# Kernel tuning notes

Measured on AMD Instinct MI355X. Metric: run time of the kernel, lower is better.

## Reference

```python
import jax, jax.numpy as jnp
import numpy as np

N = 100000   # nodes
E = 1600000  # edges
F_IN = 32    # num_features
H = 16       # hidden_size (hardcoded as conv2 input in source)
C = 10       # num_classes
K = 2        # kernel_size (dim=1)


def setup_inputs() -> dict:
    key = jax.random.key(0)
    ks = jax.random.split(key, 9)
    x = jax.random.normal(ks[0], (N, F_IN), dtype=jnp.float32)
    edge_index = jax.random.randint(ks[1], (2, E), 0, N, dtype=jnp.int64)
    edge_attr = jax.random.uniform(ks[2], (E, 1), dtype=jnp.float32)
    s1 = 1.0 / np.sqrt(F_IN)
    s2 = 1.0 / np.sqrt(H)
    W1 = jax.random.normal(ks[3], (K, F_IN, H), dtype=jnp.float32) * s1
    root1 = jax.random.normal(ks[4], (F_IN, H), dtype=jnp.float32) * s1
    b1 = jnp.zeros((H,), dtype=jnp.float32)
    W2 = jax.random.normal(ks[5], (K, H, C), dtype=jnp.float32) * s2
    root2 = jax.random.normal(ks[6], (H, C), dtype=jnp.float32) * s2
    b2 = jnp.zeros((C,), dtype=jnp.float32)
    return {"x": x, "edge_index": edge_index, "edge_attr": edge_attr,
            "W1": W1, "root1": root1, "b1": b1,
            "W2": W2, "root2": root2, "b2": b2}


def spline_conv(x, edge_index, edge_attr, W, root, bias, num_nodes):
    # Open B-spline, degree 1: hat-function basis over K knots.
    k = W.shape[0]
    src, dst = edge_index[0], edge_index[1]
    v = edge_attr[:, 0] * (k - 1)                                   # [E]
    grid = jnp.arange(k, dtype=v.dtype)
    basis = jnp.maximum(0.0, 1.0 - jnp.abs(v[:, None] - grid[None, :]))  # [E,K]
    xe = x[src]                                                      # [E,in] gather
    msg = jnp.einsum('ei,kio,ek->eo', xe, W, basis)                  # per-edge message
    agg = jax.ops.segment_sum(msg, dst, num_segments=num_nodes)      # scatter-add
    deg = jax.ops.segment_sum(jnp.ones((msg.shape[0],), x.dtype), dst,
                              num_segments=num_nodes)
    agg = agg / jnp.maximum(deg, 1.0)[:, None]                       # mean aggregation
    return agg + x @ root + bias


def reference(x, edge_index, edge_attr, W1, root1, b1, W2, root2, b2):
    # Inference mode: F.dropout(training=False) is identity.
    h = jax.nn.elu(spline_conv(x, edge_index, edge_attr, W1, root1, b1, N))
    out = spline_conv(h, edge_index, edge_attr, W2, root2, b2, N)
    return jax.nn.log_softmax(out, axis=1)
```

## Files before the change

kernel.cpp:

```cpp
#include <hip/hip_runtime.h>
#include <math.h>

#define N_NODES 100000
#define E_EDGES 1600000
#define F_IN 32
#define HID 16
#define NC 10
#define SRC_BITS 17
#define SRC_MASK ((1u << SRC_BITS) - 1u)
#define VQ_SCALE 32767.0f
#define CBITS 8
#define BUCKET_N 256
#define NCB ((N_NODES + BUCKET_N - 1) / BUCKET_N)
#define BLK_E 2048
#define NBLK ((E_EDGES + BLK_E - 1) / BLK_E)
#define NODE_GRID ((N_NODES + 255) / 256)

__device__ __forceinline__ unsigned int bf16pair(float lo, float hi) {
    unsigned int ulo = __float_as_uint(lo), uhi = __float_as_uint(hi);
    ulo += 0x7fffu + ((ulo >> 16) & 1u);
    uhi += 0x7fffu + ((uhi >> 16) & 1u);
    return (ulo >> 16) | (uhi & 0xffff0000u);
}

__device__ __forceinline__ float lerp_pair(unsigned int pair, float v) {
    float a = __uint_as_float(pair << 16);
    float b = __uint_as_float(pair & 0xffff0000u);
    return fmaf(v, b - a, a);
}

__global__ __launch_bounds__(256) void fused_l1cnt(
    const float* __restrict__ x, const float* __restrict__ W1,
    const float* __restrict__ root1, const float* __restrict__ b1,
    const int* __restrict__ ei,
    unsigned int* __restrict__ y, float* __restrict__ r1,
    int* __restrict__ cnt)
{
    if (blockIdx.x >= NODE_GRID) {
        __shared__ int h[NCB];
        int b = blockIdx.x - NODE_GRID;
        for (int i = threadIdx.x; i < NCB; i += 256) h[i] = 0;
        __syncthreads();
        const int* dstp = ei + E_EDGES;
        int e0 = b * BLK_E;
        for (int i = threadIdx.x * 4; i < BLK_E; i += 1024) {
            int e = e0 + i;
            if (e + 3 < E_EDGES) {
                int4 d4 = *(const int4*)(dstp + e);
                atomicAdd(&h[d4.x >> CBITS], 1);
                atomicAdd(&h[d4.y >> CBITS], 1);
                atomicAdd(&h[d4.z >> CBITS], 1);
                atomicAdd(&h[d4.w >> CBITS], 1);
            } else {
                for (int k = 0; k < 4; k++)
                    if (e + k < E_EDGES) atomicAdd(&h[dstp[e + k] >> CBITS], 1);
            }
        }
        __syncthreads();
        for (int s = threadIdx.x; s < NCB; s += 256)
            cnt[(size_t)s * NBLK + b] = h[s];
        return;
    }
    __shared__ float sW0[F_IN * HID], sW1[F_IN * HID], sR[F_IN * HID], sB[HID];
    for (int i = threadIdx.x; i < F_IN * HID; i += 256) {
        sW0[i] = W1[i];
        sW1[i] = W1[F_IN * HID + i];
        sR[i]  = root1[i];
    }
    if (threadIdx.x < HID) sB[threadIdx.x] = b1[threadIdx.x];
    __syncthreads();

    int n = blockIdx.x * 256 + threadIdx.x;
    if (n >= N_NODES) return;

    float xr[F_IN];
    const float4* xp = (const float4*)(x + (size_t)n * F_IN);
    #pragma unroll
    for (int i = 0; i < F_IN / 4; i++) {
        float4 t = xp[i];
        xr[i*4+0] = t.x; xr[i*4+1] = t.y; xr[i*4+2] = t.z; xr[i*4+3] = t.w;
    }

    float a0[HID], a1[HID], ar[HID];
    #pragma unroll
    for (int o = 0; o < HID; o++) { a0[o] = 0.f; a1[o] = 0.f; ar[o] = sB[o]; }
    for (int i = 0; i < F_IN; i++) {
        float xi = xr[i];
        #pragma unroll
        for (int o = 0; o < HID; o++) {
            a0[o] += xi * sW0[i * HID + o];
            a1[o] += xi * sW1[i * HID + o];
            ar[o] += xi * sR[i * HID + o];
        }
    }
    unsigned int* py = y + (size_t)n * 16;
    float* pr = r1 + (size_t)n * HID;
    #pragma unroll
    for (int o = 0; o < HID; o++) {
        py[o] = bf16pair(a0[o], a1[o]);
        pr[o] = ar[o];
    }
}

__global__ __launch_bounds__(256) void k_rowscan(
    int* __restrict__ cnt, int* __restrict__ total)
{
    __shared__ int wsum[4], woff[4];
    int s = blockIdx.x;
    int t = threadIdx.x;
    int w = t >> 6, l = t & 63;
    int carry = 0;
    int* row = cnt + (size_t)s * NBLK;
    for (int c = 0; c < NBLK; c += 256) {
        int idx = c + t;
        int v = (idx < NBLK) ? row[idx] : 0;
        int incl = v;
        #pragma unroll
        for (int off = 1; off < 64; off <<= 1) {
            int u = __shfl_up(incl, off, 64);
            if (l >= off) incl += u;
        }
        if (l == 63) wsum[w] = incl;
        __syncthreads();
        if (t == 0) {
            int a = 0;
            #pragma unroll
            for (int i = 0; i < 4; i++) { woff[i] = a; a += wsum[i]; }
        }
        __syncthreads();
        int excl = woff[w] + incl - v;
        if (idx < NBLK) row[idx] = carry + excl;
        carry += woff[3] + wsum[3];
        __syncthreads();
    }
    if (t == 0) total[s] = carry;
}

__global__ __launch_bounds__(512) void k_bucket(
    const int* __restrict__ ei, const float* __restrict__ ea,
    const int* __restrict__ cnt, const int* __restrict__ total,
    int2* __restrict__ ebuf, int* __restrict__ bb, int* __restrict__ start)
{
    __shared__ int wsum[8], woff[8];
    __shared__ int base[NCB], cur[NCB];
    int t = threadIdx.x;
    int tot = (t < NCB) ? total[t] : 0;
    int w = t >> 6, l = t & 63;
    int incl = tot;
    #pragma unroll
    for (int off = 1; off < 64; off <<= 1) {
        int u = __shfl_up(incl, off, 64);
        if (l >= off) incl += u;
    }
    if (l == 63) wsum[w] = incl;
    __syncthreads();
    if (t == 0) {
        int a = 0;
        #pragma unroll
        for (int i = 0; i < 8; i++) { woff[i] = a; a += wsum[i]; }
    }
    __syncthreads();
    int excl = woff[w] + incl - tot;
    if (t < NCB) {
        base[t] = excl + cnt[(size_t)t * NBLK + blockIdx.x];
        cur[t] = 0;
        if (blockIdx.x == 0) {
            bb[t] = excl;
            if (t == NCB - 1) { bb[NCB] = excl + tot; start[N_NODES] = E_EDGES; }
        }
    }
    __syncthreads();

    const int* dstp = ei + E_EDGES;
    int e0 = blockIdx.x * BLK_E;
    for (int i = t * 4; i < BLK_E; i += 2048) {
        int e = e0 + i;
        if (e + 3 < E_EDGES) {
            int4 d4 = *(const int4*)(dstp + e);
            int4 s4 = *(const int4*)(ei + e);
            float4 a4 = *(const float4*)(ea + e);
            {
                int s = d4.x >> CBITS;
                int off = atomicAdd(&cur[s], 1);
                unsigned int vq = (unsigned int)(a4.x * VQ_SCALE + 0.5f);
                ebuf[base[s] + off] = make_int2(d4.x & (BUCKET_N - 1),
                                               (int)((vq << SRC_BITS) | (unsigned int)s4.x));
            }
            {
                int s = d4.y >> CBITS;
                int off = atomicAdd(&cur[s], 1);
                unsigned int vq = (unsigned int)(a4.y * VQ_SCALE + 0.5f);
                ebuf[base[s] + off] = make_int2(d4.y & (BUCKET_N - 1),
                                               (int)((vq << SRC_BITS) | (unsigned int)s4.y));
            }
            {
                int s = d4.z >> CBITS;
                int off = atomicAdd(&cur[s], 1);
                unsigned int vq = (unsigned int)(a4.z * VQ_SCALE + 0.5f);
                ebuf[base[s] + off] = make_int2(d4.z & (BUCKET_N - 1),
                                               (int)((vq << SRC_BITS) | (unsigned int)s4.z));
            }
            {
                int s = d4.w >> CBITS;
                int off = atomicAdd(&cur[s], 1);
                unsigned int vq = (unsigned int)(a4.w * VQ_SCALE + 0.5f);
                ebuf[base[s] + off] = make_int2(d4.w & (BUCKET_N - 1),
                                               (int)((vq << SRC_BITS) | (unsigned int)s4.w));
            }
        } else {
            for (int k = 0; k < 4; k++) {
                int ee = e + k;
                if (ee >= E_EDGES) break;
                int dst = dstp[ee];
                int s = dst >> CBITS;
                int off = atomicAdd(&cur[s], 1);
                unsigned int vq = (unsigned int)(ea[ee] * VQ_SCALE + 0.5f);
                ebuf[base[s] + off] = make_int2(dst & (BUCKET_N - 1),
                                               (int)((vq << SRC_BITS) | (unsigned int)ei[ee]));
            }
        }
    }
}

__global__ __launch_bounds__(1024) void k_bsort(
    const int2* __restrict__ ebuf, const int* __restrict__ bb,
    unsigned int* __restrict__ es, int* __restrict__ start)
{
    __shared__ int hist[BUCKET_N];
    __shared__ int cursor[BUCKET_N];
    __shared__ int wsum[4], woff[4];
    int t = threadIdx.x;
    int b = blockIdx.x;
    int j0 = bb[b], j1 = bb[b + 1];
    if (t < BUCKET_N) { hist[t] = 0; cursor[t] = 0; }
    __syncthreads();
    for (int j = j0 + t; j < j1; j += 1024)
        atomicAdd(&hist[ebuf[j].x], 1);
    __syncthreads();
    int c = (t < BUCKET_N) ? hist[t] : 0;
    int w = t >> 6, l = t & 63;
    int incl = c;
    #pragma unroll
    for (int off = 1; off < 64; off <<= 1) {
        int u = __shfl_up(incl, off, 64);
        if (l >= off) incl += u;
    }
    if (w < 4 && l == 63) wsum[w] = incl;
    __syncthreads();
    if (t == 0) {
        int acc = 0;
        #pragma unroll
        for (int i = 0; i < 4; i++) { woff[i] = acc; acc += wsum[i]; }
    }
    __syncthreads();
    if (t < BUCKET_N) {
        int excl = woff[w] + incl - c;
        hist[t] = excl;
        int node = (b << CBITS) + t;
        if (node < N_NODES) start[node] = j0 + excl;
    }
    __syncthreads();
    for (int j = j0 + t; j < j1; j += 1024) {
        int2 p = ebuf[j];
        int off = atomicAdd(&cursor[p.x], 1);
        es[j0 + hist[p.x] + off] = (unsigned int)p.y;
    }
}

__global__ __launch_bounds__(256) void k_agg1(
    const unsigned int* __restrict__ es, const int* __restrict__ start,
    const unsigned int* __restrict__ y, const float* __restrict__ r1,
    const float* __restrict__ W2, const float* __restrict__ root2,
    const float* __restrict__ b2,
    unsigned int* __restrict__ z, float* __restrict__ r2)
{
    __shared__ float sh[16 * 17];
    __shared__ float sW0[HID * NC], sW1[HID * NC], sRt[HID * NC], sB2[NC];
    int t = threadIdx.x;
    if (t < HID * NC) { sW0[t] = W2[t]; sW1[t] = W2[HID * NC + t]; sRt[t] = root2[t]; }
    if (t >= HID * NC && t < HID * NC + NC) sB2[t - HID * NC] = b2[t - HID * NC];

    int idx = blockIdx.x * 256 + t;
    int n = idx >> 4, o = idx & 15, g = t >> 4;
    if (n < N_NODES) {
        int j0 = start[n], j1 = start[n + 1];
        float acc0 = 0.f, acc1 = 0.f, acc2 = 0.f, acc3 = 0.f;
        int j = j0;
        for (; j + 7 < j1; j += 8) {
            unsigned int p0 = es[j],   p1 = es[j+1], p2 = es[j+2], p3 = es[j+3];
            unsigned int p4 = es[j+4], p5 = es[j+5], p6 = es[j+6], p7 = es[j+7];
            unsigned int q0 = y[(size_t)(p0 & SRC_MASK) * 16 + o];
            unsigned int q1 = y[(size_t)(p1 & SRC_MASK) * 16 + o];
            unsigned int q2 = y[(size_t)(p2 & SRC_MASK) * 16 + o];
            unsigned int q3 = y[(size_t)(p3 & SRC_MASK) * 16 + o];
            unsigned int q4 = y[(size_t)(p4 & SRC_MASK) * 16 + o];
            unsigned int q5 = y[(size_t)(p5 & SRC_MASK) * 16 + o];
            unsigned int q6 = y[(size_t)(p6 & SRC_MASK) * 16 + o];
            unsigned int q7 = y[(size_t)(p7 & SRC_MASK) * 16 + o];
            acc0 += lerp_pair(q0, (float)(p0 >> SRC_BITS) * (1.0f / VQ_SCALE));
            acc1 += lerp_pair(q1, (float)(p1 >> SRC_BITS) * (1.0f / VQ_SCALE));
            acc2 += lerp_pair(q2, (float)(p2 >> SRC_BITS) * (1.0f / VQ_SCALE));
            acc3 += lerp_pair(q3, (float)(p3 >> SRC_BITS) * (1.0f / VQ_SCALE));
            acc0 += lerp_pair(q4, (float)(p4 >> SRC_BITS) * (1.0f / VQ_SCALE));
            acc1 += lerp_pair(q5, (float)(p5 >> SRC_BITS) * (1.0f / VQ_SCALE));
            acc2 += lerp_pair(q6, (float)(p6 >> SRC_BITS) * (1.0f / VQ_SCALE));
            acc3 += lerp_pair(q7, (float)(p7 >> SRC_BITS) * (1.0f / VQ_SCALE));
        }
        for (; j + 3 < j1; j += 4) {
            unsigned int p0 = es[j], p1 = es[j+1], p2 = es[j+2], p3 = es[j+3];
            unsigned int q0 = y[(size_t)(p0 & SRC_MASK) * 16 + o];
            unsigned int q1 = y[(size_t)(p1 & SRC_MASK) * 16 + o];
            unsigned int q2 = y[(size_t)(p2 & SRC_MASK) * 16 + o];
            unsigned int q3 = y[(size_t)(p3 & SRC_MASK) * 16 + o];
            acc0 += lerp_pair(q0, (float)(p0 >> SRC_BITS) * (1.0f / VQ_SCALE));
            acc1 += lerp_pair(q1, (float)(p1 >> SRC_BITS) * (1.0f / VQ_SCALE));
            acc2 += lerp_pair(q2, (float)(p2 >> SRC_BITS) * (1.0f / VQ_SCALE));
            acc3 += lerp_pair(q3, (float)(p3 >> SRC_BITS) * (1.0f / VQ_SCALE));
        }
        for (; j < j1; j++) {
            unsigned int p = es[j];
            unsigned int q = y[(size_t)(p & SRC_MASK) * 16 + o];
            acc0 += lerp_pair(q, (float)(p >> SRC_BITS) * (1.0f / VQ_SCALE));
        }
        float acc = (acc0 + acc1) + (acc2 + acc3);
        float inv = 1.0f / fmaxf((float)(j1 - j0), 1.0f);
        float hv = acc * inv + r1[(size_t)n * HID + o];
        sh[g * 17 + o] = hv > 0.0f ? hv : expm1f(hv);
    }
    __syncthreads();

    int n2 = blockIdx.x * 16 + g;
    if (n2 < N_NODES) {
        int cc = o;
        unsigned int* pz = z + (size_t)n2 * 16;
        if (cc < NC) {
            float a0 = 0.f, a1 = 0.f, ar = sB2[cc];
            #pragma unroll
            for (int i = 0; i < HID; i++) {
                float hi = sh[g * 17 + i];
                a0 += hi * sW0[i * NC + cc];
                a1 += hi * sW1[i * NC + cc];
                ar += hi * sRt[i * NC + cc];
            }
            pz[cc] = bf16pair(a0, a1);
            r2[(size_t)n2 * NC + cc] = ar;
        } else {
            pz[cc] = 0u;
        }
    }
}

__global__ __launch_bounds__(256) void k_agg2(
    const unsigned int* __restrict__ es, const int* __restrict__ start,
    const unsigned int* __restrict__ z,
    const float* __restrict__ r2, float* __restrict__ out)
{
    int idx = blockIdx.x * 256 + threadIdx.x;
    int n = idx >> 4, o = idx & 15;
    if (n >= N_NODES) return;
    int j0 = start[n], j1 = start[n + 1];
    float acc0 = 0.f, acc1 = 0.f, acc2 = 0.f, acc3 = 0.f;
    int j = j0;
    for (; j + 7 < j1; j += 8) {
        unsigned int p0 = es[j],   p1 = es[j+1], p2 = es[j+2], p3 = es[j+3];
        unsigned int p4 = es[j+4], p5 = es[j+5], p6 = es[j+6], p7 = es[j+7];
        unsigned int q0 = z[(size_t)(p0 & SRC_MASK) * 16 + o];
        unsigned int q1 = z[(size_t)(p1 & SRC_MASK) * 16 + o];
        unsigned int q2 = z[(size_t)(p2 & SRC_MASK) * 16 + o];
        unsigned int q3 = z[(size_t)(p3 & SRC_MASK) * 16 + o];
        unsigned int q4 = z[(size_t)(p4 & SRC_MASK) * 16 + o];
        unsigned int q5 = z[(size_t)(p5 & SRC_MASK) * 16 + o];
        unsigned int q6 = z[(size_t)(p6 & SRC_MASK) * 16 + o];
        unsigned int q7 = z[(size_t)(p7 & SRC_MASK) * 16 + o];
        acc0 += lerp_pair(q0, (float)(p0 >> SRC_BITS) * (1.0f / VQ_SCALE));
        acc1 += lerp_pair(q1, (float)(p1 >> SRC_BITS) * (1.0f / VQ_SCALE));
        acc2 += lerp_pair(q2, (float)(p2 >> SRC_BITS) * (1.0f / VQ_SCALE));
        acc3 += lerp_pair(q3, (float)(p3 >> SRC_BITS) * (1.0f / VQ_SCALE));
        acc0 += lerp_pair(q4, (float)(p4 >> SRC_BITS) * (1.0f / VQ_SCALE));
        acc1 += lerp_pair(q5, (float)(p5 >> SRC_BITS) * (1.0f / VQ_SCALE));
        acc2 += lerp_pair(q6, (float)(p6 >> SRC_BITS) * (1.0f / VQ_SCALE));
        acc3 += lerp_pair(q7, (float)(p7 >> SRC_BITS) * (1.0f / VQ_SCALE));
    }
    for (; j + 3 < j1; j += 4) {
        unsigned int p0 = es[j], p1 = es[j+1], p2 = es[j+2], p3 = es[j+3];
        unsigned int q0 = z[(size_t)(p0 & SRC_MASK) * 16 + o];
        unsigned int q1 = z[(size_t)(p1 & SRC_MASK) * 16 + o];
        unsigned int q2 = z[(size_t)(p2 & SRC_MASK) * 16 + o];
        unsigned int q3 = z[(size_t)(p3 & SRC_MASK) * 16 + o];
        acc0 += lerp_pair(q0, (float)(p0 >> SRC_BITS) * (1.0f / VQ_SCALE));
        acc1 += lerp_pair(q1, (float)(p1 >> SRC_BITS) * (1.0f / VQ_SCALE));
        acc2 += lerp_pair(q2, (float)(p2 >> SRC_BITS) * (1.0f / VQ_SCALE));
        acc3 += lerp_pair(q3, (float)(p3 >> SRC_BITS) * (1.0f / VQ_SCALE));
    }
    for (; j < j1; j++) {
        unsigned int p = es[j];
        unsigned int q = z[(size_t)(p & SRC_MASK) * 16 + o];
        acc0 += lerp_pair(q, (float)(p >> SRC_BITS) * (1.0f / VQ_SCALE));
    }
    float acc = (acc0 + acc1) + (acc2 + acc3);
    float val = -INFINITY;
    if (o < NC) {
        float inv = 1.0f / fmaxf((float)(j1 - j0), 1.0f);
        val = acc * inv + r2[(size_t)n * NC + o];
    }
    float mx = val;
    #pragma unroll
    for (int off = 8; off > 0; off >>= 1) mx = fmaxf(mx, __shfl_xor(mx, off, 16));
    float ex = (o < NC) ? expf(val - mx) : 0.0f;
    float ssum = ex;
    #pragma unroll
    for (int off = 8; off > 0; off >>= 1) ssum += __shfl_xor(ssum, off, 16);
    if (o < NC) out[(size_t)n * NC + o] = val - mx - logf(ssum);
}

extern "C" void kernel_launch(void* const* d_in, const int* in_sizes, int n_in,
                              void* d_out, int out_size, void* d_ws, size_t ws_size,
                              hipStream_t stream) {
    const float* x     = (const float*)d_in[0];
    const int*   ei    = (const int*)d_in[1];
    const float* ea    = (const float*)d_in[2];
    const float* W1    = (const float*)d_in[3];
    const float* root1 = (const float*)d_in[4];
    const float* b1    = (const float*)d_in[5];
    const float* W2    = (const float*)d_in[6];
    const float* root2 = (const float*)d_in[7];
    const float* b2    = (const float*)d_in[8];
    float* out = (float*)d_out;

    char* wsb = (char*)d_ws;
    int2*         ebuf   = (int2*)wsb;
    unsigned int* es     = (unsigned int*)(wsb + (size_t)E_EDGES * 8);
    unsigned int* y      = es + (size_t)E_EDGES;
    float*        r1     = (float*)(y + (size_t)N_NODES * 16);
    unsigned int* z      = (unsigned int*)(r1 + (size_t)N_NODES * HID);
    float*        r2     = (float*)(z + (size_t)N_NODES * 16);
    int*          start  = (int*)(r2 + (size_t)N_NODES * NC);
    int*          cnt    = start + N_NODES + 1;
    int*          total  = cnt + (size_t)NCB * NBLK;
    int*          bb     = total + NCB;

    int aggGrid  = (N_NODES * 16 + 255) / 256;

    fused_l1cnt<<<NODE_GRID + NBLK, 256, 0, stream>>>(x, W1, root1, b1, ei, y, r1, cnt);
    k_rowscan<<<NCB, 256, 0, stream>>>(cnt, total);
    k_bucket<<<NBLK, 512, 0, stream>>>(ei, ea, cnt, total, ebuf, bb, start);
    k_bsort <<<NCB, 1024, 0, stream>>>(ebuf, bb, es, start);
    k_agg1  <<<aggGrid, 256, 0, stream>>>(es, start, y, r1, W2, root2, b2, z, r2);
    k_agg2  <<<aggGrid, 256, 0, stream>>>(es, start, z, r2, out);
}
```

Before: 185.5 us.

## Drop per-node CSR sort; aggregate each destination bucket in shared memory

```diff
diff --git a/kernel.cpp b/kernel.cpp
--- a/kernel.cpp
+++ b/kernel.cpp
@@ -9,8 +9,8 @@
 #define SRC_BITS 17
 #define SRC_MASK ((1u << SRC_BITS) - 1u)
 #define VQ_SCALE 32767.0f
-#define CBITS 8
-#define BUCKET_N 256
+#define CBITS 7
+#define BUCKET_N 128
 #define NCB ((N_NODES + BUCKET_N - 1) / BUCKET_N)
 #define BLK_E 2048
 #define NBLK ((E_EDGES + BLK_E - 1) / BLK_E)
@@ -139,36 +139,40 @@
 __global__ __launch_bounds__(512) void k_bucket(
     const int* __restrict__ ei, const float* __restrict__ ea,
     const int* __restrict__ cnt, const int* __restrict__ total,
-    int2* __restrict__ ebuf, int* __restrict__ bb, int* __restrict__ start)
+    int2* __restrict__ ebuf, int* __restrict__ bb)
 {
     __shared__ int wsum[8], woff[8];
     __shared__ int base[NCB], cur[NCB];
     int t = threadIdx.x;
-    int tot = (t < NCB) ? total[t] : 0;
     int w = t >> 6, l = t & 63;
-    int incl = tot;
-    #pragma unroll
-    for (int off = 1; off < 64; off <<= 1) {
-        int u = __shfl_up(incl, off, 64);
-        if (l >= off) incl += u;
-    }
-    if (l == 63) wsum[w] = incl;
-    __syncthreads();
-    if (t == 0) {
-        int a = 0;
-        #pragma unroll
-        for (int i = 0; i < 8; i++) { woff[i] = a; a += wsum[i]; }
-    }
-    __syncthreads();
-    int excl = woff[w] + incl - tot;
-    if (t < NCB) {
-        base[t] = excl + cnt[(size_t)t * NBLK + blockIdx.x];
-        cur[t] = 0;
-        if (blockIdx.x == 0) {
-            bb[t] = excl;
-            if (t == NCB - 1) { bb[NCB] = excl + tot; start[N_NODES] = E_EDGES; }
-        }
-    }
+    int carry = 0;
+    for (int c = 0; c < NCB; c += 512) {
+        int idx = c + t;
+        int v = (idx < NCB) ? total[idx] : 0;
+        int incl = v;
+        #pragma unroll
+        for (int off = 1; off < 64; off <<= 1) {
+            int u = __shfl_up(incl, off, 64);
+            if (l >= off) incl += u;
+        }
+        if (l == 63) wsum[w] = incl;
+        __syncthreads();
+        if (t == 0) {
+            int a = 0;
+            #pragma unroll
+            for (int i = 0; i < 8; i++) { woff[i] = a; a += wsum[i]; }
+        }
+        __syncthreads();
+        if (idx < NCB) {
+            int excl = carry + woff[w] + incl - v;
+            base[idx] = excl + cnt[(size_t)idx * NBLK + blockIdx.x];
+            cur[idx] = 0;
+            if (blockIdx.x == 0) bb[idx] = excl;
+        }
+        carry += woff[7] + wsum[7];
+        __syncthreads();
+    }
+    if (blockIdx.x == 0 && t == 0) bb[NCB] = carry;
     __syncthreads();
 
     const int* dstp = ei + E_EDGES;
@@ -222,195 +226,109 @@
     }
 }
 
-__global__ __launch_bounds__(1024) void k_bsort(
+__global__ __launch_bounds__(512) void k_bagg1(
     const int2* __restrict__ ebuf, const int* __restrict__ bb,
-    unsigned int* __restrict__ es, int* __restrict__ start)
-{
-    __shared__ int hist[BUCKET_N];
-    __shared__ int cursor[BUCKET_N];
-    __shared__ int wsum[4], woff[4];
-    int t = threadIdx.x;
-    int b = blockIdx.x;
-    int j0 = bb[b], j1 = bb[b + 1];
-    if (t < BUCKET_N) { hist[t] = 0; cursor[t] = 0; }
-    __syncthreads();
-    for (int j = j0 + t; j < j1; j += 1024)
-        atomicAdd(&hist[ebuf[j].x], 1);
-    __syncthreads();
-    int c = (t < BUCKET_N) ? hist[t] : 0;
-    int w = t >> 6, l = t & 63;
-    int incl = c;
-    #pragma unroll
-    for (int off = 1; off < 64; off <<= 1) {
-        int u = __shfl_up(incl, off, 64);
-        if (l >= off) incl += u;
-    }
-    if (w < 4 && l == 63) wsum[w] = incl;
-    __syncthreads();
-    if (t == 0) {
-        int acc = 0;
-        #pragma unroll
-        for (int i = 0; i < 4; i++) { woff[i] = acc; acc += wsum[i]; }
-    }
-    __syncthreads();
-    if (t < BUCKET_N) {
-        int excl = woff[w] + incl - c;
-        hist[t] = excl;
-        int node = (b << CBITS) + t;
-        if (node < N_NODES) start[node] = j0 + excl;
-    }
-    __syncthreads();
-    for (int j = j0 + t; j < j1; j += 1024) {
-        int2 p = ebuf[j];
-        int off = atomicAdd(&cursor[p.x], 1);
-        es[j0 + hist[p.x] + off] = (unsigned int)p.y;
-    }
-}
-
-__global__ __launch_bounds__(256) void k_agg1(
-    const unsigned int* __restrict__ es, const int* __restrict__ start,
     const unsigned int* __restrict__ y, const float* __restrict__ r1,
     const float* __restrict__ W2, const float* __restrict__ root2,
     const float* __restrict__ b2,
-    unsigned int* __restrict__ z, float* __restrict__ r2)
-{
-    __shared__ float sh[16 * 17];
+    unsigned int* __restrict__ z, float* __restrict__ r2,
+    float* __restrict__ invdeg)
+{
+    __shared__ float acc[BUCKET_N * 16];
+    __shared__ int sdeg[BUCKET_N];
     __shared__ float sW0[HID * NC], sW1[HID * NC], sRt[HID * NC], sB2[NC];
     int t = threadIdx.x;
+    int b = blockIdx.x;
+    for (int i = t; i < BUCKET_N * 16; i += 512) acc[i] = 0.f;
+    if (t < BUCKET_N) sdeg[t] = 0;
     if (t < HID * NC) { sW0[t] = W2[t]; sW1[t] = W2[HID * NC + t]; sRt[t] = root2[t]; }
     if (t >= HID * NC && t < HID * NC + NC) sB2[t - HID * NC] = b2[t - HID * NC];
-
-    int idx = blockIdx.x * 256 + t;
-    int n = idx >> 4, o = idx & 15, g = t >> 4;
-    if (n < N_NODES) {
-        int j0 = start[n], j1 = start[n + 1];
-        float acc0 = 0.f, acc1 = 0.f, acc2 = 0.f, acc3 = 0.f;
-        int j = j0;
-        for (; j + 7 < j1; j += 8) {
-            unsigned int p0 = es[j],   p1 = es[j+1], p2 = es[j+2], p3 = es[j+3];
-            unsigned int p4 = es[j+4], p5 = es[j+5], p6 = es[j+6], p7 = es[j+7];
-            unsigned int q0 = y[(size_t)(p0 & SRC_MASK) * 16 + o];
-            unsigned int q1 = y[(size_t)(p1 & SRC_MASK) * 16 + o];
-            unsigned int q2 = y[(size_t)(p2 & SRC_MASK) * 16 + o];
-            unsigned int q3 = y[(size_t)(p3 & SRC_MASK) * 16 + o];
-            unsigned int q4 = y[(size_t)(p4 & SRC_MASK) * 16 + o];
-            unsigned int q5 = y[(size_t)(p5 & SRC_MASK) * 16 + o];
-            unsigned int q6 = y[(size_t)(p6 & SRC_MASK) * 16 + o];
-            unsigned int q7 = y[(size_t)(p7 & SRC_MASK) * 16 + o];
-            acc0 += lerp_pair(q0, (float)(p0 >> SRC_BITS) * (1.0f / VQ_SCALE));
-            acc1 += lerp_pair(q1, (float)(p1 >> SRC_BITS) * (1.0f / VQ_SCALE));
-            acc2 += lerp_pair(q2, (float)(p2 >> SRC_BITS) * (1.0f / VQ_SCALE));
-            acc3 += lerp_pair(q3, (float)(p3 >> SRC_BITS) * (1.0f / VQ_SCALE));
-            acc0 += lerp_pair(q4, (float)(p4 >> SRC_BITS) * (1.0f / VQ_SCALE));
-            acc1 += lerp_pair(q5, (float)(p5 >> SRC_BITS) * (1.0f / VQ_SCALE));
-            acc2 += lerp_pair(q6, (float)(p6 >> SRC_BITS) * (1.0f / VQ_SCALE));
-            acc3 += lerp_pair(q7, (float)(p7 >> SRC_BITS) * (1.0f / VQ_SCALE));
-        }
-        for (; j + 3 < j1; j += 4) {
-            unsigned int p0 = es[j], p1 = es[j+1], p2 = es[j+2], p3 = es[j+3];
-            unsigned int q0 = y[(size_t)(p0 & SRC_MASK) * 16 + o];
-            unsigned int q1 = y[(size_t)(p1 & SRC_MASK) * 16 + o];
-            unsigned int q2 = y[(size_t)(p2 & SRC_MASK) * 16 + o];
-            unsigned int q3 = y[(size_t)(p3 & SRC_MASK) * 16 + o];
-            acc0 += lerp_pair(q0, (float)(p0 >> SRC_BITS) * (1.0f / VQ_SCALE));
-            acc1 += lerp_pair(q1, (float)(p1 >> SRC_BITS) * (1.0f / VQ_SCALE));
-            acc2 += lerp_pair(q2, (float)(p2 >> SRC_BITS) * (1.0f / VQ_SCALE));
-            acc3 += lerp_pair(q3, (float)(p3 >> SRC_BITS) * (1.0f / VQ_SCALE));
-        }
-        for (; j < j1; j++) {
-            unsigned int p = es[j];
-            unsigned int q = y[(size_t)(p & SRC_MASK) * 16 + o];
-            acc0 += lerp_pair(q, (float)(p >> SRC_BITS) * (1.0f / VQ_SCALE));
-        }
-        float acc = (acc0 + acc1) + (acc2 + acc3);
-        float inv = 1.0f / fmaxf((float)(j1 - j0), 1.0f);
-        float hv = acc * inv + r1[(size_t)n * HID + o];
-        sh[g * 17 + o] = hv > 0.0f ? hv : expm1f(hv);
-    }
-    __syncthreads();
-
-    int n2 = blockIdx.x * 16 + g;
-    if (n2 < N_NODES) {
-        int cc = o;
-        unsigned int* pz = z + (size_t)n2 * 16;
-        if (cc < NC) {
-            float a0 = 0.f, a1 = 0.f, ar = sB2[cc];
-            #pragma unroll
-            for (int i = 0; i < HID; i++) {
-                float hi = sh[g * 17 + i];
-                a0 += hi * sW0[i * NC + cc];
-                a1 += hi * sW1[i * NC + cc];
-                ar += hi * sRt[i * NC + cc];
-            }
-            pz[cc] = bf16pair(a0, a1);
-            r2[(size_t)n2 * NC + cc] = ar;
-        } else {
-            pz[cc] = 0u;
-        }
-    }
-}
-
-__global__ __launch_bounds__(256) void k_agg2(
-    const unsigned int* __restrict__ es, const int* __restrict__ start,
-    const unsigned int* __restrict__ z,
-    const float* __restrict__ r2, float* __restrict__ out)
-{
-    int idx = blockIdx.x * 256 + threadIdx.x;
-    int n = idx >> 4, o = idx & 15;
-    if (n >= N_NODES) return;
-    int j0 = start[n], j1 = start[n + 1];
-    float acc0 = 0.f, acc1 = 0.f, acc2 = 0.f, acc3 = 0.f;
-    int j = j0;
-    for (; j + 7 < j1; j += 8) {
-        unsigned int p0 = es[j],   p1 = es[j+1], p2 = es[j+2], p3 = es[j+3];
-        unsigned int p4 = es[j+4], p5 = es[j+5], p6 = es[j+6], p7 = es[j+7];
-        unsigned int q0 = z[(size_t)(p0 & SRC_MASK) * 16 + o];
-        unsigned int q1 = z[(size_t)(p1 & SRC_MASK) * 16 + o];
-        unsigned int q2 = z[(size_t)(p2 & SRC_MASK) * 16 + o];
-        unsigned int q3 = z[(size_t)(p3 & SRC_MASK) * 16 + o];
-        unsigned int q4 = z[(size_t)(p4 & SRC_MASK) * 16 + o];
-        unsigned int q5 = z[(size_t)(p5 & SRC_MASK) * 16 + o];
-        unsigned int q6 = z[(size_t)(p6 & SRC_MASK) * 16 + o];
-        unsigned int q7 = z[(size_t)(p7 & SRC_MASK) * 16 + o];
-        acc0 += lerp_pair(q0, (float)(p0 >> SRC_BITS) * (1.0f / VQ_SCALE));
-        acc1 += lerp_pair(q1, (float)(p1 >> SRC_BITS) * (1.0f / VQ_SCALE));
-        acc2 += lerp_pair(q2, (float)(p2 >> SRC_BITS) * (1.0f / VQ_SCALE));
-        acc3 += lerp_pair(q3, (float)(p3 >> SRC_BITS) * (1.0f / VQ_SCALE));
-        acc0 += lerp_pair(q4, (float)(p4 >> SRC_BITS) * (1.0f / VQ_SCALE));
-        acc1 += lerp_pair(q5, (float)(p5 >> SRC_BITS) * (1.0f / VQ_SCALE));
-        acc2 += lerp_pair(q6, (float)(p6 >> SRC_BITS) * (1.0f / VQ_SCALE));
-        acc3 += lerp_pair(q7, (float)(p7 >> SRC_BITS) * (1.0f / VQ_SCALE));
-    }
-    for (; j + 3 < j1; j += 4) {
-        unsigned int p0 = es[j], p1 = es[j+1], p2 = es[j+2], p3 = es[j+3];
-        unsigned int q0 = z[(size_t)(p0 & SRC_MASK) * 16 + o];
-        unsigned int q1 = z[(size_t)(p1 & SRC_MASK) * 16 + o];
-        unsigned int q2 = z[(size_t)(p2 & SRC_MASK) * 16 + o];
-        unsigned int q3 = z[(size_t)(p3 & SRC_MASK) * 16 + o];
-        acc0 += lerp_pair(q0, (float)(p0 >> SRC_BITS) * (1.0f / VQ_SCALE));
-        acc1 += lerp_pair(q1, (float)(p1 >> SRC_BITS) * (1.0f / VQ_SCALE));
-        acc2 += lerp_pair(q2, (float)(p2 >> SRC_BITS) * (1.0f / VQ_SCALE));
-        acc3 += lerp_pair(q3, (float)(p3 >> SRC_BITS) * (1.0f / VQ_SCALE));
-    }
-    for (; j < j1; j++) {
-        unsigned int p = es[j];
-        unsigned int q = z[(size_t)(p & SRC_MASK) * 16 + o];
-        acc0 += lerp_pair(q, (float)(p >> SRC_BITS) * (1.0f / VQ_SCALE));
-    }
-    float acc = (acc0 + acc1) + (acc2 + acc3);
-    float val = -INFINITY;
-    if (o < NC) {
-        float inv = 1.0f / fmaxf((float)(j1 - j0), 1.0f);
-        val = acc * inv + r2[(size_t)n * NC + o];
-    }
-    float mx = val;
-    #pragma unroll
-    for (int off = 8; off > 0; off >>= 1) mx = fmaxf(mx, __shfl_xor(mx, off, 16));
-    float ex = (o < NC) ? expf(val - mx) : 0.0f;
-    float ssum = ex;
-    #pragma unroll
-    for (int off = 8; off > 0; off >>= 1) ssum += __shfl_xor(ssum, off, 16);
-    if (o < NC) out[(size_t)n * NC + o] = val - mx - logf(ssum);
+    __syncthreads();
+
+    int j0 = bb[b], j1 = bb[b + 1];
+    int o = t & 15;
+    #pragma unroll 4
+    for (int j = j0 + (t >> 4); j < j1; j += 32) {
+        int2 p = ebuf[j];
+        unsigned int pe = (unsigned int)p.y;
+        float v = (float)(pe >> SRC_BITS) * (1.0f / VQ_SCALE);
+        unsigned int q = y[(size_t)(pe & SRC_MASK) * 16 + o];
+        atomicAdd(&acc[p.x * 16 + o], lerp_pair(q, v));
+        if (o == 0) atomicAdd(&sdeg[p.x], 1);
+    }
+    __syncthreads();
+
+    for (int n = t >> 4; n < BUCKET_N; n += 32) {
+        int node = b * BUCKET_N + n;
+        if (node < N_NODES) {
+            float inv = 1.0f / fmaxf((float)sdeg[n], 1.0f);
+            float hv = acc[n * 16 + o] * inv + r1[(size_t)node * HID + o];
+            acc[n * 16 + o] = hv > 0.0f ? hv : expm1f(hv);
+            if (o == 0) invdeg[node] = inv;
+        }
+    }
+    __syncthreads();
+
+    for (int n = t >> 4; n < BUCKET_N; n += 32) {
+        int node = b * BUCKET_N + n;
+        if (node < N_NODES) {
+            unsigned int* pz = z + (size_t)node * 16;
+            if (o < NC) {
+                float a0 = 0.f, a1 = 0.f, ar = sB2[o];
+                #pragma unroll
+                for (int i = 0; i < HID; i++) {
+                    float hi = acc[n * 16 + i];
+                    a0 += hi * sW0[i * NC + o];
+                    a1 += hi * sW1[i * NC + o];
+                    ar += hi * sRt[i * NC + o];
+                }
+                pz[o] = bf16pair(a0, a1);
+                r2[(size_t)node * NC + o] = ar;
+            } else {
+                pz[o] = 0u;
+            }
+        }
+    }
+}
+
+__global__ __launch_bounds__(512) void k_bagg2(
+    const int2* __restrict__ ebuf, const int* __restrict__ bb,
+    const unsigned int* __restrict__ z, const float* __restrict__ r2,
+    const float* __restrict__ invdeg, float* __restrict__ out)
+{
+    __shared__ float acc[BUCKET_N * 16];
+    int t = threadIdx.x;
+    int b = blockIdx.x;
+    for (int i = t; i < BUCKET_N * 16; i += 512) acc[i] = 0.f;
+    __syncthreads();
+
+    int j0 = bb[b], j1 = bb[b + 1];
+    int o = t & 15;
+    #pragma unroll 4
+    for (int j = j0 + (t >> 4); j < j1; j += 32) {
+        int2 p = ebuf[j];
+        unsigned int pe = (unsigned int)p.y;
+        float v = (float)(pe >> SRC_BITS) * (1.0f / VQ_SCALE);
+        unsigned int q = z[(size_t)(pe & SRC_MASK) * 16 + o];
+        atomicAdd(&acc[p.x * 16 + o], lerp_pair(q, v));
+    }
+    __syncthreads();
+
+    for (int n = t >> 4; n < BUCKET_N; n += 32) {
+        int node = b * BUCKET_N + n;
+        if (node >= N_NODES) continue;
+        float val = -INFINITY;
+        if (o < NC)
+            val = acc[n * 16 + o] * invdeg[node] + r2[(size_t)node * NC + o];
+        float mx = val;
+        #pragma unroll
+        for (int off = 8; off > 0; off >>= 1) mx = fmaxf(mx, __shfl_xor(mx, off, 16));
+        float ex = (o < NC) ? expf(val - mx) : 0.0f;
+        float ssum = ex;
+        #pragma unroll
+        for (int off = 8; off > 0; off >>= 1) ssum += __shfl_xor(ssum, off, 16);
+        if (o < NC) out[(size_t)node * NC + o] = val - mx - logf(ssum);
+    }
 }
 
 extern "C" void kernel_launch(void* const* d_in, const int* in_sizes, int n_in,
@@ -429,22 +347,18 @@
 
     char* wsb = (char*)d_ws;
     int2*         ebuf   = (int2*)wsb;
-    unsigned int* es     = (unsigned int*)(wsb + (size_t)E_EDGES * 8);
-    unsigned int* y      = es + (size_t)E_EDGES;
+    unsigned int* y      = (unsigned int*)(wsb + (size_t)E_EDGES * 8);
     float*        r1     = (float*)(y + (size_t)N_NODES * 16);
     unsigned int* z      = (unsigned int*)(r1 + (size_t)N_NODES * HID);
     float*        r2     = (float*)(z + (size_t)N_NODES * 16);
-    int*          start  = (int*)(r2 + (size_t)N_NODES * NC);
-    int*          cnt    = start + N_NODES + 1;
+    float*        invdeg = r2 + (size_t)N_NODES * NC;
+    int*          cnt    = (int*)(invdeg + N_NODES);
     int*          total  = cnt + (size_t)NCB * NBLK;
     int*          bb     = total + NCB;
 
-    int aggGrid  = (N_NODES * 16 + 255) / 256;
-
     fused_l1cnt<<<NODE_GRID + NBLK, 256, 0, stream>>>(x, W1, root1, b1, ei, y, r1, cnt);
     k_rowscan<<<NCB, 256, 0, stream>>>(cnt, total);
-    k_bucket<<<NBLK, 512, 0, stream>>>(ei, ea, cnt, total, ebuf, bb, start);
-    k_bsort <<<NCB, 1024, 0, stream>>>(ebuf, bb, es, start);
-    k_agg1  <<<aggGrid, 256, 0, stream>>>(es, start, y, r1, W2, root2, b2, z, r2);
-    k_agg2  <<<aggGrid, 256, 0, stream>>>(es, start, z, r2, out);
-}
+    k_bucket<<<NBLK, 512, 0, stream>>>(ei, ea, cnt, total, ebuf, bb);
+    k_bagg1 <<<NCB, 512, 0, stream>>>(ebuf, bb, y, r1, W2, root2, b2, z, r2, invdeg);
+    k_bagg2 <<<NCB, 512, 0, stream>>>(ebuf, bb, z, r2, invdeg, out);
+}
```

New measurement: 491.2 us. +164.8%, slower.

## Use 4 threads per node with 16-byte vector gathers in aggregation kernels

Applied to the files above, without the earlier changes.

```diff
diff --git a/kernel.cpp b/kernel.cpp
--- a/kernel.cpp
+++ b/kernel.cpp
@@ -274,79 +274,86 @@
     const float* __restrict__ b2,
     unsigned int* __restrict__ z, float* __restrict__ r2)
 {
-    __shared__ float sh[16 * 17];
     __shared__ float sW0[HID * NC], sW1[HID * NC], sRt[HID * NC], sB2[NC];
     int t = threadIdx.x;
     if (t < HID * NC) { sW0[t] = W2[t]; sW1[t] = W2[HID * NC + t]; sRt[t] = root2[t]; }
     if (t >= HID * NC && t < HID * NC + NC) sB2[t - HID * NC] = b2[t - HID * NC];
+    __syncthreads();
 
     int idx = blockIdx.x * 256 + t;
-    int n = idx >> 4, o = idx & 15, g = t >> 4;
-    if (n < N_NODES) {
-        int j0 = start[n], j1 = start[n + 1];
-        float acc0 = 0.f, acc1 = 0.f, acc2 = 0.f, acc3 = 0.f;
-        int j = j0;
-        for (; j + 7 < j1; j += 8) {
-            unsigned int p0 = es[j],   p1 = es[j+1], p2 = es[j+2], p3 = es[j+3];
-            unsigned int p4 = es[j+4], p5 = es[j+5], p6 = es[j+6], p7 = es[j+7];
-            unsigned int q0 = y[(size_t)(p0 & SRC_MASK) * 16 + o];
-            unsigned int q1 = y[(size_t)(p1 & SRC_MASK) * 16 + o];
-            unsigned int q2 = y[(size_t)(p2 & SRC_MASK) * 16 + o];
-            unsigned int q3 = y[(size_t)(p3 & SRC_MASK) * 16 + o];
-            unsigned int q4 = y[(size_t)(p4 & SRC_MASK) * 16 + o];
-            unsigned int q5 = y[(size_t)(p5 & SRC_MASK) * 16 + o];
-            unsigned int q6 = y[(size_t)(p6 & SRC_MASK) * 16 + o];
-            unsigned int q7 = y[(size_t)(p7 & SRC_MASK) * 16 + o];
-            acc0 += lerp_pair(q0, (float)(p0 >> SRC_BITS) * (1.0f / VQ_SCALE));
-            acc1 += lerp_pair(q1, (float)(p1 >> SRC_BITS) * (1.0f / VQ_SCALE));
-            acc2 += lerp_pair(q2, (float)(p2 >> SRC_BITS) * (1.0f / VQ_SCALE));
-            acc3 += lerp_pair(q3, (float)(p3 >> SRC_BITS) * (1.0f / VQ_SCALE));
-            acc0 += lerp_pair(q4, (float)(p4 >> SRC_BITS) * (1.0f / VQ_SCALE));
-            acc1 += lerp_pair(q5, (float)(p5 >> SRC_BITS) * (1.0f / VQ_SCALE));
-            acc2 += lerp_pair(q6, (float)(p6 >> SRC_BITS) * (1.0f / VQ_SCALE));
-            acc3 += lerp_pair(q7, (float)(p7 >> SRC_BITS) * (1.0f / VQ_SCALE));
-        }
-        for (; j + 3 < j1; j += 4) {
-            unsigned int p0 = es[j], p1 = es[j+1], p2 = es[j+2], p3 = es[j+3];
-            unsigned int q0 = y[(size_t)(p0 & SRC_MASK) * 16 + o];
-            unsigned int q1 = y[(size_t)(p1 & SRC_MASK) * 16 + o];
-            unsigned int q2 = y[(size_t)(p2 & SRC_MASK) * 16 + o];
-            unsigned int q3 = y[(size_t)(p3 & SRC_MASK) * 16 + o];
-            acc0 += lerp_pair(q0, (float)(p0 >> SRC_BITS) * (1.0f / VQ_SCALE));
-            acc1 += lerp_pair(q1, (float)(p1 >> SRC_BITS) * (1.0f / VQ_SCALE));
-            acc2 += lerp_pair(q2, (float)(p2 >> SRC_BITS) * (1.0f / VQ_SCALE));
-            acc3 += lerp_pair(q3, (float)(p3 >> SRC_BITS) * (1.0f / VQ_SCALE));
-        }
-        for (; j < j1; j++) {
-            unsigned int p = es[j];
-            unsigned int q = y[(size_t)(p & SRC_MASK) * 16 + o];
-            acc0 += lerp_pair(q, (float)(p >> SRC_BITS) * (1.0f / VQ_SCALE));
-        }
-        float acc = (acc0 + acc1) + (acc2 + acc3);
-        float inv = 1.0f / fmaxf((float)(j1 - j0), 1.0f);
-        float hv = acc * inv + r1[(size_t)n * HID + o];
-        sh[g * 17 + o] = hv > 0.0f ? hv : expm1f(hv);
-    }
-    __syncthreads();
-
-    int n2 = blockIdx.x * 16 + g;
-    if (n2 < N_NODES) {
-        int cc = o;
-        unsigned int* pz = z + (size_t)n2 * 16;
-        if (cc < NC) {
-            float a0 = 0.f, a1 = 0.f, ar = sB2[cc];
+    int n = idx >> 2, l = idx & 3;
+    if (n >= N_NODES) return;
+    int j0 = start[n], j1 = start[n + 1];
+    const uint4* yrow = (const uint4*)y;
+    float acc[4] = {0.f, 0.f, 0.f, 0.f};
+    int j = j0;
+    for (; j + 3 < j1; j += 4) {
+        unsigned int p0 = es[j], p1 = es[j+1], p2 = es[j+2], p3 = es[j+3];
+        uint4 q0 = yrow[(size_t)(p0 & SRC_MASK) * 4 + l];
+        uint4 q1 = yrow[(size_t)(p1 & SRC_MASK) * 4 + l];
+        uint4 q2 = yrow[(size_t)(p2 & SRC_MASK) * 4 + l];
+        uint4 q3 = yrow[(size_t)(p3 & SRC_MASK) * 4 + l];
+        float v0 = (float)(p0 >> SRC_BITS) * (1.0f / VQ_SCALE);
+        float v1 = (float)(p1 >> SRC_BITS) * (1.0f / VQ_SCALE);
+        float v2 = (float)(p2 >> SRC_BITS) * (1.0f / VQ_SCALE);
+        float v3 = (float)(p3 >> SRC_BITS) * (1.0f / VQ_SCALE);
+        acc[0] += lerp_pair(q0.x, v0); acc[1] += lerp_pair(q0.y, v0);
+        acc[2] += lerp_pair(q0.z, v0); acc[3] += lerp_pair(q0.w, v0);
+        acc[0] += lerp_pair(q1.x, v1); acc[1] += lerp_pair(q1.y, v1);
+        acc[2] += lerp_pair(q1.z, v1); acc[3] += lerp_pair(q1.w, v1);
+        acc[0] += lerp_pair(q2.x, v2); acc[1] += lerp_pair(q2.y, v2);
+        acc[2] += lerp_pair(q2.z, v2); acc[3] += lerp_pair(q2.w, v2);
+        acc[0] += lerp_pair(q3.x, v3); acc[1] += lerp_pair(q3.y, v3);
+        acc[2] += lerp_pair(q3.z, v3); acc[3] += lerp_pair(q3.w, v3);
+    }
+    for (; j < j1; j++) {
+        unsigned int p = es[j];
+        uint4 q = yrow[(size_t)(p & SRC_MASK) * 4 + l];
+        float v = (float)(p >> SRC_BITS) * (1.0f / VQ_SCALE);
+        acc[0] += lerp_pair(q.x, v); acc[1] += lerp_pair(q.y, v);
+        acc[2] += lerp_pair(q.z, v); acc[3] += lerp_pair(q.w, v);
+    }
+    float inv = 1.0f / fmaxf((float)(j1 - j0), 1.0f);
+    float4 rr = *(const float4*)(r1 + (size_t)n * HID + l * 4);
+    float hv[4];
+    hv[0] = acc[0] * inv + rr.x;
+    hv[1] = acc[1] * inv + rr.y;
+    hv[2] = acc[2] * inv + rr.z;
+    hv[3] = acc[3] * inv + rr.w;
+    #pragma unroll
+    for (int e = 0; e < 4; e++) hv[e] = hv[e] > 0.0f ? hv[e] : expm1f(hv[e]);
+
+    int cbase = l * 4;
+    float a0[4] = {0.f, 0.f, 0.f, 0.f}, a1[4] = {0.f, 0.f, 0.f, 0.f}, ar[4];
+    #pragma unroll
+    for (int e = 0; e < 4; e++) { int c = cbase + e; ar[e] = (c < NC) ? sB2[c] : 0.f; }
+    #pragma unroll
+    for (int s = 0; s < 4; s++) {
+        #pragma unroll
+        for (int e2 = 0; e2 < 4; e2++) {
+            float hi = __shfl(hv[e2], s, 4);
+            int i = s * 4 + e2;
             #pragma unroll
-            for (int i = 0; i < HID; i++) {
-                float hi = sh[g * 17 + i];
-                a0 += hi * sW0[i * NC + cc];
-                a1 += hi * sW1[i * NC + cc];
-                ar += hi * sRt[i * NC + cc];
-            }
-            pz[cc] = bf16pair(a0, a1);
-            r2[(size_t)n2 * NC + cc] = ar;
-        } else {
-            pz[cc] = 0u;
-        }
+            for (int e = 0; e < 4; e++) {
+                int c = cbase + e;
+                if (c < NC) {
+                    a0[e] += hi * sW0[i * NC + c];
+                    a1[e] += hi * sW1[i * NC + c];
+                    ar[e] += hi * sRt[i * NC + c];
+                }
+            }
+        }
+    }
+    uint4 zo;
+    zo.x = (cbase + 0 < NC) ? bf16pair(a0[0], a1[0]) : 0u;
+    zo.y = (cbase + 1 < NC) ? bf16pair(a0[1], a1[1]) : 0u;
+    zo.z = (cbase + 2 < NC) ? bf16pair(a0[2], a1[2]) : 0u;
+    zo.w = (cbase + 3 < NC) ? bf16pair(a0[3], a1[3]) : 0u;
+    ((uint4*)z)[(size_t)n * 4 + l] = zo;
+    #pragma unroll
+    for (int e = 0; e < 4; e++) {
+        int c = cbase + e;
+        if (c < NC) r2[(size_t)n * NC + c] = ar[e];
     }
 }
 
@@ -356,61 +363,63 @@
     const float* __restrict__ r2, float* __restrict__ out)
 {
     int idx = blockIdx.x * 256 + threadIdx.x;
-    int n = idx >> 4, o = idx & 15;
+    int n = idx >> 2, l = idx & 3;
     if (n >= N_NODES) return;
     int j0 = start[n], j1 = start[n + 1];
-    float acc0 = 0.f, acc1 = 0.f, acc2 = 0.f, acc3 = 0.f;
+    const uint4* zrow = (const uint4*)z;
+    float acc[4] = {0.f, 0.f, 0.f, 0.f};
     int j = j0;
-    for (; j + 7 < j1; j += 8) {
-        unsigned int p0 = es[j],   p1 = es[j+1], p2 = es[j+2], p3 = es[j+3];
-        unsigned int p4 = es[j+4], p5 = es[j+5], p6 = es[j+6], p7 = es[j+7];
-        unsigned int q0 = z[(size_t)(p0 & SRC_MASK) * 16 + o];
-        unsigned int q1 = z[(size_t)(p1 & SRC_MASK) * 16 + o];
-        unsigned int q2 = z[(size_t)(p2 & SRC_MASK) * 16 + o];
-        unsigned int q3 = z[(size_t)(p3 & SRC_MASK) * 16 + o];
-        unsigned int q4 = z[(size_t)(p4 & SRC_MASK) * 16 + o];
-        unsigned int q5 = z[(size_t)(p5 & SRC_MASK) * 16 + o];
-        unsigned int q6 = z[(size_t)(p6 & SRC_MASK) * 16 + o];
-        unsigned int q7 = z[(size_t)(p7 & SRC_MASK) * 16 + o];
-        acc0 += lerp_pair(q0, (float)(p0 >> SRC_BITS) * (1.0f / VQ_SCALE));
-        acc1 += lerp_pair(q1, (float)(p1 >> SRC_BITS) * (1.0f / VQ_SCALE));
-        acc2 += lerp_pair(q2, (float)(p2 >> SRC_BITS) * (1.0f / VQ_SCALE));
-        acc3 += lerp_pair(q3, (float)(p3 >> SRC_BITS) * (1.0f / VQ_SCALE));
-        acc0 += lerp_pair(q4, (float)(p4 >> SRC_BITS) * (1.0f / VQ_SCALE));
-        acc1 += lerp_pair(q5, (float)(p5 >> SRC_BITS) * (1.0f / VQ_SCALE));
-        acc2 += lerp_pair(q6, (float)(p6 >> SRC_BITS) * (1.0f / VQ_SCALE));
-        acc3 += lerp_pair(q7, (float)(p7 >> SRC_BITS) * (1.0f / VQ_SCALE));
-    }
     for (; j + 3 < j1; j += 4) {
         unsigned int p0 = es[j], p1 = es[j+1], p2 = es[j+2], p3 = es[j+3];
-        unsigned int q0 = z[(size_t)(p0 & SRC_MASK) * 16 + o];
-        unsigned int q1 = z[(size_t)(p1 & SRC_MASK) * 16 + o];
-        unsigned int q2 = z[(size_t)(p2 & SRC_MASK) * 16 + o];
-        unsigned int q3 = z[(size_t)(p3 & SRC_MASK) * 16 + o];
-        acc0 += lerp_pair(q0, (float)(p0 >> SRC_BITS) * (1.0f / VQ_SCALE));
-        acc1 += lerp_pair(q1, (float)(p1 >> SRC_BITS) * (1.0f / VQ_SCALE));
-        acc2 += lerp_pair(q2, (float)(p2 >> SRC_BITS) * (1.0f / VQ_SCALE));
-        acc3 += lerp_pair(q3, (float)(p3 >> SRC_BITS) * (1.0f / VQ_SCALE));
+        uint4 q0 = zrow[(size_t)(p0 & SRC_MASK) * 4 + l];
+        uint4 q1 = zrow[(size_t)(p1 & SRC_MASK) * 4 + l];
+        uint4 q2 = zrow[(size_t)(p2 & SRC_MASK) * 4 + l];
+        uint4 q3 = zrow[(size_t)(p3 & SRC_MASK) * 4 + l];
+        float v0 = (float)(p0 >> SRC_BITS) * (1.0f / VQ_SCALE);
+        float v1 = (float)(p1 >> SRC_BITS) * (1.0f / VQ_SCALE);
+        float v2 = (float)(p2 >> SRC_BITS) * (1.0f / VQ_SCALE);
+        float v3 = (float)(p3 >> SRC_BITS) * (1.0f / VQ_SCALE);
+        acc[0] += lerp_pair(q0.x, v0); acc[1] += lerp_pair(q0.y, v0);
+        acc[2] += lerp_pair(q0.z, v0); acc[3] += lerp_pair(q0.w, v0);
+        acc[0] += lerp_pair(q1.x, v1); acc[1] += lerp_pair(q1.y, v1);
+        acc[2] += lerp_pair(q1.z, v1); acc[3] += lerp_pair(q1.w, v1);
+        acc[0] += lerp_pair(q2.x, v2); acc[1] += lerp_pair(q2.y, v2);
+        acc[2] += lerp_pair(q2.z, v2); acc[3] += lerp_pair(q2.w, v2);
+        acc[0] += lerp_pair(q3.x, v3); acc[1] += lerp_pair(q3.y, v3);
+        acc[2] += lerp_pair(q3.z, v3); acc[3] += lerp_pair(q3.w, v3);
     }
     for (; j < j1; j++) {
         unsigned int p = es[j];
-        unsigned int q = z[(size_t)(p & SRC_MASK) * 16 + o];
-        acc0 += lerp_pair(q, (float)(p >> SRC_BITS) * (1.0f / VQ_SCALE));
-    }
-    float acc = (acc0 + acc1) + (acc2 + acc3);
-    float val = -INFINITY;
-    if (o < NC) {
-        float inv = 1.0f / fmaxf((float)(j1 - j0), 1.0f);
-        val = acc * inv + r2[(size_t)n * NC + o];
-    }
-    float mx = val;
-    #pragma unroll
-    for (int off = 8; off > 0; off >>= 1) mx = fmaxf(mx, __shfl_xor(mx, off, 16));
-    float ex = (o < NC) ? expf(val - mx) : 0.0f;
-    float ssum = ex;
-    #pragma unroll
-    for (int off = 8; off > 0; off >>= 1) ssum += __shfl_xor(ssum, off, 16);
-    if (o < NC) out[(size_t)n * NC + o] = val - mx - logf(ssum);
+        uint4 q = zrow[(size_t)(p & SRC_MASK) * 4 + l];
+        float v = (float)(p >> SRC_BITS) * (1.0f / VQ_SCALE);
+        acc[0] += lerp_pair(q.x, v); acc[1] += lerp_pair(q.y, v);
+        acc[2] += lerp_pair(q.z, v); acc[3] += lerp_pair(q.w, v);
+    }
+    float inv = 1.0f / fmaxf((float)(j1 - j0), 1.0f);
+    int cbase = l * 4;
+    float val[4];
+    #pragma unroll
+    for (int e = 0; e < 4; e++) {
+        int c = cbase + e;
+        val[e] = (c < NC) ? acc[e] * inv + r2[(size_t)n * NC + c] : -INFINITY;
+    }
+    float mx = fmaxf(fmaxf(val[0], val[1]), fmaxf(val[2], val[3]));
+    mx = fmaxf(mx, __shfl_xor(mx, 1, 4));
+    mx = fmaxf(mx, __shfl_xor(mx, 2, 4));
+    float ssum = 0.f;
+    #pragma unroll
+    for (int e = 0; e < 4; e++) {
+        int c = cbase + e;
+        if (c < NC) ssum += expf(val[e] - mx);
+    }
+    ssum += __shfl_xor(ssum, 1, 4);
+    ssum += __shfl_xor(ssum, 2, 4);
+    float lse = logf(ssum);
+    #pragma unroll
+    for (int e = 0; e < 4; e++) {
+        int c = cbase + e;
+        if (c < NC) out[(size_t)n * NC + c] = val[e] - mx - lse;
+    }
 }
 
 extern "C" void kernel_launch(void* const* d_in, const int* in_sizes, int n_in,
@@ -439,7 +448,7 @@
     int*          total  = cnt + (size_t)NCB * NBLK;
     int*          bb     = total + NCB;
 
-    int aggGrid  = (N_NODES * 16 + 255) / 256;
+    int aggGrid = (N_NODES * 4 + 255) / 256;
 
     fused_l1cnt<<<NODE_GRID + NBLK, 256, 0, stream>>>(x, W1, root1, b1, ei, y, r1, cnt);
     k_rowscan<<<NCB, 256, 0, stream>>>(cnt, total);
```

New measurement: 180.7 us. 1.03x faster.
